# Optimization experiments

Measured on AMD Instinct MI355X. Metric: run time of the kernel, lower is better.

The kernel has to match this reference:

```python
import jax, jax.numpy as jnp
import numpy as np

N_CH = 64          # n_channels
N_HID = 64         # int(ratio * n_inputs), ratio=1, log_diag_cov -> n_inputs = n_channels
N_OUT_CH = 64      # n_out_channels defaults to n_channels
N_MLP_OUT = N_OUT_CH * (N_CH + 1)  # 4160


def setup_inputs() -> dict:
    key = jax.random.key(0)
    k0, k1, k2, k3, k4 = jax.random.split(key, 5)
    x = jax.random.normal(k0, (256, 1, N_CH, 4000), dtype=jnp.float32)
    W1 = jax.random.normal(k1, (N_CH, N_HID), dtype=jnp.float32) * 0.05
    b1 = jax.random.normal(k2, (N_HID,), dtype=jnp.float32) * 0.05
    W2 = jax.random.normal(k3, (N_HID, N_MLP_OUT), dtype=jnp.float32) * 0.05
    b2 = jax.random.normal(k4, (N_MLP_OUT,), dtype=jnp.float32) * 0.05
    return {"x": x, "W1": W1, "b1": b1, "W2": W2, "b2": b2}


def reference(x, W1, b1, W2, b2):
    # x: (B, F, C, T)
    b, f, c, t = x.shape
    # SpatialFeatureExtractor('log_diag_cov'): log of unbiased variance over T
    v = jnp.var(x, axis=3, ddof=1)               # (B, F, C)
    feats = jnp.log(v)
    feats = jnp.where(jnp.isneginf(feats), 0.0, feats)
    # two-layer MLP hypernetwork
    h = jax.nn.relu(feats @ W1 + b1)             # (B, F, H)
    mlp_out = h @ W2 + b2                        # (B, F, n_out_ch*(C+1))
    bias = mlp_out[:, :, :N_OUT_CH].reshape(b, f, N_OUT_CH, 1)
    W = mlp_out[:, :, N_OUT_CH:].reshape(b, f, N_OUT_CH, c)
    # per-sample spatial filter: batched matmul + bias
    out = jnp.einsum('bfoc,bfct->bfot', W, x) + bias  # (B, F, C', T)
    return out.squeeze(1)                        # squeeze_dim1=True, F=1
```

## Files before the change

kernel.cpp:

```cpp
#include <hip/hip_runtime.h>
#include <hip/hip_bf16.h>
#include <cstdint>
#include <math.h>

#define BB 256
#define CC 64
#define TT 4000
#define NHID 64
#define NOUT 64
#define NMLP (NOUT*(CC+1))
#define TCH 128

typedef __attribute__((ext_vector_type(8))) short short8v;
typedef __attribute__((ext_vector_type(4))) float f32x4;

__global__ __launch_bounds__(1024) void k_feat(const float* __restrict__ x,
                                               const float* __restrict__ W1,
                                               const float* __restrict__ b1,
                                               const float* __restrict__ W2,
                                               const float* __restrict__ b2,
                                               __hip_bfloat16* __restrict__ wtg,
                                               float* __restrict__ wsB) {
    int b   = blockIdx.x;
    int tid = threadIdx.x;
    int c   = tid >> 4;
    int sub = tid & 15;

    const float4* row = (const float4*)(x + (size_t)b * (CC * TT) + (size_t)c * TT);
    float s = 0.f, ss = 0.f;
    #pragma unroll 4
    for (int i = sub; i < TT / 4; i += 16) {
        float4 v = row[i];
        s  += v.x + v.y + v.z + v.w;
        ss += v.x * v.x + v.y * v.y + v.z * v.z + v.w * v.w;
    }
    #pragma unroll
    for (int off = 8; off > 0; off >>= 1) {
        s  += __shfl_xor(s, off);
        ss += __shfl_xor(ss, off);
    }

    __shared__ float fs[CC];
    __shared__ float hs[NHID];
    if (sub == 0) {
        float var = (ss - s * s / (float)TT) / (float)(TT - 1);
        float f = logf(var);
        if (isinf(f) && f < 0.f) f = 0.f;
        fs[c] = f;
    }
    __syncthreads();

    if (tid < NHID) {
        float v = b1[tid];
        #pragma unroll 8
        for (int k = 0; k < CC; ++k) v = fmaf(fs[k], W1[k * NHID + tid], v);
        hs[tid] = v > 0.f ? v : 0.f;
    }
    __syncthreads();

    for (int j = tid; j < NMLP; j += 1024) {
        float v = b2[j];
        #pragma unroll 8
        for (int k = 0; k < NHID; ++k) v = fmaf(hs[k], W2[k * NMLP + j], v);
        if (j < NOUT) {
            wsB[b * NOUT + j] = v;
        } else {
            wtg[(size_t)b * 4096 + (j - NOUT)] = __float2bfloat16(v);
        }
    }
}

__global__ __launch_bounds__(256, 4) void k_apply(const float* __restrict__ x,
                                                  const __hip_bfloat16* __restrict__ wtg,
                                                  const float* __restrict__ wsB,
                                                  float* __restrict__ out) {
    int b   = (BB - 1) - blockIdx.y;
    int tb  = blockIdx.x * TCH;
    int tid = threadIdx.x;
    int l   = tid & 63, w = tid >> 6;

    __shared__ unsigned short xt[2][TCH * CC];

    int cslot = tid & 7;
    int f4    = tid >> 3;
    int maxf4 = ((TT - tb) >> 2) - 1;
    int f4c   = f4 <= maxf4 ? f4 : maxf4;
    const float* xb = x + (size_t)b * (CC * TT) + tb + f4c * 4;

    float4 xr[8];
    #pragma unroll
    for (int p = 0; p < 8; ++p)
        xr[p] = *(const float4*)(xb + (size_t)(cslot * 8 + p) * TT);

    #pragma unroll
    for (int j = 0; j < 4; ++j) {
        int t = f4 * 4 + j;
        short8v hv, lv;
        #pragma unroll
        for (int p = 0; p < 8; ++p) {
            float v = (&xr[p].x)[j];
            __hip_bfloat16 h = __float2bfloat16(v);
            unsigned short hu = *(unsigned short*)&h;
            float hf = __uint_as_float((unsigned)hu << 16);
            __hip_bfloat16 lo = __float2bfloat16(v - hf);
            hv[p] = (short)hu;
            lv[p] = (short)*(unsigned short*)&lo;
        }
        int byteoff = t * 128 + ((cslot * 16) ^ ((t & 7) << 4));
        *(short8v*)((char*)&xt[0][0] + byteoff) = hv;
        *(short8v*)((char*)&xt[1][0] + byteoff) = lv;
    }
    __syncthreads();

    const __hip_bfloat16* wb = wtg + (size_t)b * 4096;
    short8v af[4][2];
    #pragma unroll
    for (int mi = 0; mi < 4; ++mi)
        #pragma unroll
        for (int kc = 0; kc < 2; ++kc)
            af[mi][kc] = *(const short8v*)(wb + (mi * 16 + (l & 15)) * 64
                                              + kc * 32 + (l >> 4) * 8);

    f32x4 acc[4][2];
    #pragma unroll
    for (int mi = 0; mi < 4; ++mi) {
        float4 bv = *(const float4*)(wsB + b * 64 + mi * 16 + (l >> 4) * 4);
        #pragma unroll
        for (int ti = 0; ti < 2; ++ti) {
            acc[mi][ti][0] = bv.x; acc[mi][ti][1] = bv.y;
            acc[mi][ti][2] = bv.z; acc[mi][ti][3] = bv.w;
        }
    }

    #pragma unroll
    for (int ti = 0; ti < 2; ++ti) {
        int tl = w * 32 + ti * 16 + (l & 15);
        int rowbase = tl * 128;
        int sw = (tl & 7) << 4;
        short8v bf[2][2];
        #pragma unroll
        for (int kc = 0; kc < 2; ++kc) {
            int boff = rowbase + ((kc * 64 + (l >> 4) * 16) ^ sw);
            bf[kc][0] = *(const short8v*)((const char*)&xt[0][0] + boff);
            bf[kc][1] = *(const short8v*)((const char*)&xt[1][0] + boff);
        }
        #pragma unroll
        for (int mi = 0; mi < 4; ++mi)
            #pragma unroll
            for (int kc = 0; kc < 2; ++kc) {
                acc[mi][ti] = __builtin_amdgcn_mfma_f32_16x16x32_bf16(
                                  af[mi][kc], bf[kc][0], acc[mi][ti], 0, 0, 0);
                acc[mi][ti] = __builtin_amdgcn_mfma_f32_16x16x32_bf16(
                                  af[mi][kc], bf[kc][1], acc[mi][ti], 0, 0, 0);
            }
    }

    __syncthreads();
    float* ot = (float*)&xt[0][0];

    #pragma unroll
    for (int mi = 0; mi < 4; ++mi)
        #pragma unroll
        for (int ti = 0; ti < 2; ++ti) {
            int t = w * 32 + ti * 16 + (l & 15);
            #pragma unroll
            for (int r = 0; r < 4; ++r) {
                int o = mi * 16 + (l >> 4) * 4 + r;
                ot[o * 128 + (t ^ ((o & 7) << 2))] = acc[mi][ti][r];
            }
        }
    __syncthreads();

    int ro = tid >> 3;
    int q0 = tid & 7;
    #pragma unroll
    for (int k2 = 0; k2 < 2; ++k2) {
        int o = ro + k2 * 32;
        int sw = (o & 7) << 2;
        float* op = out + (size_t)b * (NOUT * TT) + (size_t)o * TT + tb;
        #pragma unroll
        for (int kq = 0; kq < 4; ++kq) {
            int t0 = (q0 + kq * 8) * 4;
            if (tb + t0 < TT) {
                f32x4 v = *(const f32x4*)&ot[o * 128 + (t0 ^ sw)];
                __builtin_nontemporal_store(v, (f32x4*)(op + t0));
            }
        }
    }
}

extern "C" void kernel_launch(void* const* d_in, const int* in_sizes, int n_in,
                              void* d_out, int out_size, void* d_ws, size_t ws_size,
                              hipStream_t stream) {
    const float* x  = (const float*)d_in[0];
    const float* W1 = (const float*)d_in[1];
    const float* b1 = (const float*)d_in[2];
    const float* W2 = (const float*)d_in[3];
    const float* b2 = (const float*)d_in[4];
    float* out = (float*)d_out;
    float* ws  = (float*)d_ws;

    float*           wsB = ws;
    __hip_bfloat16*  wtg = (__hip_bfloat16*)(ws + 16384);

    k_feat<<<256, 1024, 0, stream>>>(x, W1, b1, W2, b2, wtg, wsB);
    k_apply<<<dim3(32, 256), 256, 0, stream>>>(x, wtg, wsB, out);
}
```

Measured before the change: 150.3 us.

## Fuse feature MLP and spatial filter apply into one per-batch kernel

Merges the variance/MLP kernel and the MFMA apply kernel into a single 1024-thread block per batch sample. The generated filter weights and bias stay in shared memory instead of going through a global workspace, and four 256-thread sub-groups loop over time chunks, re-reading x that may still be in cache. This removes one launch and the workspace round trip, but it shrinks the grid from 8192 blocks to 256 and uses much more LDS per block, which lowers occupancy and latency hiding.

After: 217.3 us. +44.6%, slower.

```diff
diff --git a/kernel.cpp b/kernel.cpp
--- a/kernel.cpp
+++ b/kernel.cpp
@@ -14,39 +14,43 @@
 typedef __attribute__((ext_vector_type(8))) short short8v;
 typedef __attribute__((ext_vector_type(4))) float f32x4;
 
-__global__ __launch_bounds__(1024) void k_feat(const float* __restrict__ x,
-                                               const float* __restrict__ W1,
-                                               const float* __restrict__ b1,
-                                               const float* __restrict__ W2,
-                                               const float* __restrict__ b2,
-                                               __hip_bfloat16* __restrict__ wtg,
-                                               float* __restrict__ wsB) {
+__global__ __launch_bounds__(1024) void k_fused(const float* __restrict__ x,
+                                                const float* __restrict__ W1,
+                                                const float* __restrict__ b1,
+                                                const float* __restrict__ W2,
+                                                const float* __restrict__ b2,
+                                                float* __restrict__ out) {
     int b   = blockIdx.x;
     int tid = threadIdx.x;
-    int c   = tid >> 4;
-    int sub = tid & 15;
-
-    const float4* row = (const float4*)(x + (size_t)b * (CC * TT) + (size_t)c * TT);
-    float s = 0.f, ss = 0.f;
-    #pragma unroll 4
-    for (int i = sub; i < TT / 4; i += 16) {
-        float4 v = row[i];
-        s  += v.x + v.y + v.z + v.w;
-        ss += v.x * v.x + v.y * v.y + v.z * v.z + v.w * v.w;
-    }
-    #pragma unroll
-    for (int off = 8; off > 0; off >>= 1) {
-        s  += __shfl_xor(s, off);
-        ss += __shfl_xor(ss, off);
-    }
-
+
+    __shared__ unsigned short xt[4][2][TCH * CC];
+    __shared__ unsigned short wl[4096];
+    __shared__ float bl[64];
     __shared__ float fs[CC];
     __shared__ float hs[NHID];
-    if (sub == 0) {
-        float var = (ss - s * s / (float)TT) / (float)(TT - 1);
-        float f = logf(var);
-        if (isinf(f) && f < 0.f) f = 0.f;
-        fs[c] = f;
+
+    {
+        int c   = tid >> 4;
+        int sub = tid & 15;
+        const float4* row = (const float4*)(x + (size_t)b * (CC * TT) + (size_t)c * TT);
+        float s = 0.f, ss = 0.f;
+        #pragma unroll 4
+        for (int i = sub; i < TT / 4; i += 16) {
+            float4 v = row[i];
+            s  += v.x + v.y + v.z + v.w;
+            ss += v.x * v.x + v.y * v.y + v.z * v.z + v.w * v.w;
+        }
+        #pragma unroll
+        for (int off = 8; off > 0; off >>= 1) {
+            s  += __shfl_xor(s, off);
+            ss += __shfl_xor(ss, off);
+        }
+        if (sub == 0) {
+            float var = (ss - s * s / (float)TT) / (float)(TT - 1);
+            float f = logf(var);
+            if (isinf(f) && f < 0.f) f = 0.f;
+            fs[c] = f;
+        }
     }
     __syncthreads();
 
@@ -57,135 +61,140 @@
         hs[tid] = v > 0.f ? v : 0.f;
     }
     __syncthreads();
-
     for (int j = tid; j < NMLP; j += 1024) {
         float v = b2[j];
         #pragma unroll 8
         for (int k = 0; k < NHID; ++k) v = fmaf(hs[k], W2[k * NMLP + j], v);
         if (j < NOUT) {
-            wsB[b * NOUT + j] = v;
+            bl[j] = v;
         } else {
-            wtg[(size_t)b * 4096 + (j - NOUT)] = __float2bfloat16(v);
-        }
-    }
-}
-
-__global__ __launch_bounds__(256, 4) void k_apply(const float* __restrict__ x,
-                                                  const __hip_bfloat16* __restrict__ wtg,
-                                                  const float* __restrict__ wsB,
-                                                  float* __restrict__ out) {
-    int b   = (BB - 1) - blockIdx.y;
-    int tb  = blockIdx.x * TCH;
-    int tid = threadIdx.x;
-    int l   = tid & 63, w = tid >> 6;
-
-    __shared__ unsigned short xt[2][TCH * CC];
-
-    int cslot = tid & 7;
-    int f4    = tid >> 3;
-    int maxf4 = ((TT - tb) >> 2) - 1;
-    int f4c   = f4 <= maxf4 ? f4 : maxf4;
-    const float* xb = x + (size_t)b * (CC * TT) + tb + f4c * 4;
-
-    float4 xr[8];
-    #pragma unroll
-    for (int p = 0; p < 8; ++p)
-        xr[p] = *(const float4*)(xb + (size_t)(cslot * 8 + p) * TT);
-
-    #pragma unroll
-    for (int j = 0; j < 4; ++j) {
-        int t = f4 * 4 + j;
-        short8v hv, lv;
-        #pragma unroll
-        for (int p = 0; p < 8; ++p) {
-            float v = (&xr[p].x)[j];
+            int o = (j - NOUT) >> 6, c = (j - NOUT) & 63;
             __hip_bfloat16 h = __float2bfloat16(v);
-            unsigned short hu = *(unsigned short*)&h;
-            float hf = __uint_as_float((unsigned)hu << 16);
-            __hip_bfloat16 lo = __float2bfloat16(v - hf);
-            hv[p] = (short)hu;
-            lv[p] = (short)*(unsigned short*)&lo;
-        }
-        int byteoff = t * 128 + ((cslot * 16) ^ ((t & 7) << 4));
-        *(short8v*)((char*)&xt[0][0] + byteoff) = hv;
-        *(short8v*)((char*)&xt[1][0] + byteoff) = lv;
+            int byte = o * 128 + ((2 * c) ^ ((o & 7) << 4));
+            *(unsigned short*)((char*)wl + byte) = *(unsigned short*)&h;
+        }
     }
     __syncthreads();
 
-    const __hip_bfloat16* wb = wtg + (size_t)b * 4096;
+    int sb    = tid >> 8;
+    int stid  = tid & 255;
+    int l     = stid & 63;
+    int w     = stid >> 6;
+    int cslot = stid & 7;
+    int f4    = stid >> 3;
+
     short8v af[4][2];
     #pragma unroll
     for (int mi = 0; mi < 4; ++mi)
         #pragma unroll
-        for (int kc = 0; kc < 2; ++kc)
-            af[mi][kc] = *(const short8v*)(wb + (mi * 16 + (l & 15)) * 64
-                                              + kc * 32 + (l >> 4) * 8);
-
-    f32x4 acc[4][2];
-    #pragma unroll
-    for (int mi = 0; mi < 4; ++mi) {
-        float4 bv = *(const float4*)(wsB + b * 64 + mi * 16 + (l >> 4) * 4);
-        #pragma unroll
-        for (int ti = 0; ti < 2; ++ti) {
-            acc[mi][ti][0] = bv.x; acc[mi][ti][1] = bv.y;
-            acc[mi][ti][2] = bv.z; acc[mi][ti][3] = bv.w;
-        }
-    }
-
-    #pragma unroll
-    for (int ti = 0; ti < 2; ++ti) {
-        int tl = w * 32 + ti * 16 + (l & 15);
-        int rowbase = tl * 128;
-        int sw = (tl & 7) << 4;
-        short8v bf[2][2];
-        #pragma unroll
         for (int kc = 0; kc < 2; ++kc) {
-            int boff = rowbase + ((kc * 64 + (l >> 4) * 16) ^ sw);
-            bf[kc][0] = *(const short8v*)((const char*)&xt[0][0] + boff);
-            bf[kc][1] = *(const short8v*)((const char*)&xt[1][0] + boff);
-        }
-        #pragma unroll
-        for (int mi = 0; mi < 4; ++mi)
-            #pragma unroll
-            for (int kc = 0; kc < 2; ++kc) {
-                acc[mi][ti] = __builtin_amdgcn_mfma_f32_16x16x32_bf16(
-                                  af[mi][kc], bf[kc][0], acc[mi][ti], 0, 0, 0);
-                acc[mi][ti] = __builtin_amdgcn_mfma_f32_16x16x32_bf16(
-                                  af[mi][kc], bf[kc][1], acc[mi][ti], 0, 0, 0);
-            }
-    }
-
-    __syncthreads();
-    float* ot = (float*)&xt[0][0];
-
+            int o = mi * 16 + (l & 15);
+            int colbyte = kc * 64 + (l >> 4) * 16;
+            af[mi][kc] = *(const short8v*)((const char*)wl
+                             + o * 128 + (colbyte ^ ((o & 7) << 4)));
+        }
+    float4 bvr[4];
     #pragma unroll
     for (int mi = 0; mi < 4; ++mi)
+        bvr[mi] = *(const float4*)&bl[mi * 16 + (l >> 4) * 4];
+
+    unsigned short* xts = &xt[sb][0][0];
+    unsigned short* xtl = &xt[sb][1][0];
+    float*          ot  = (float*)&xt[sb][0][0];
+
+    #pragma unroll 1
+    for (int it = 0; it < 8; ++it) {
+        int tb = (it * 4 + sb) * TCH;
+
+        int maxf4 = ((TT - tb) >> 2) - 1;
+        int f4c   = f4 <= maxf4 ? f4 : maxf4;
+        const float* xb = x + (size_t)b * (CC * TT) + tb + f4c * 4;
+        float4 xr[8];
+        #pragma unroll
+        for (int p = 0; p < 8; ++p)
+            xr[p] = *(const float4*)(xb + (size_t)(cslot * 8 + p) * TT);
+        #pragma unroll
+        for (int j = 0; j < 4; ++j) {
+            int t = f4 * 4 + j;
+            short8v hv, lv;
+            #pragma unroll
+            for (int p = 0; p < 8; ++p) {
+                float v = (&xr[p].x)[j];
+                __hip_bfloat16 h = __float2bfloat16(v);
+                unsigned short hu = *(unsigned short*)&h;
+                float hf = __uint_as_float((unsigned)hu << 16);
+                __hip_bfloat16 lo2 = __float2bfloat16(v - hf);
+                hv[p] = (short)hu;
+                lv[p] = (short)*(unsigned short*)&lo2;
+            }
+            int byteoff = t * 128 + ((cslot * 16) ^ ((t & 7) << 4));
+            *(short8v*)((char*)xts + byteoff) = hv;
+            *(short8v*)((char*)xtl + byteoff) = lv;
+        }
+        __syncthreads();
+
+        f32x4 acc[4][2];
+        #pragma unroll
+        for (int mi = 0; mi < 4; ++mi)
+            #pragma unroll
+            for (int ti = 0; ti < 2; ++ti) {
+                acc[mi][ti][0] = bvr[mi].x; acc[mi][ti][1] = bvr[mi].y;
+                acc[mi][ti][2] = bvr[mi].z; acc[mi][ti][3] = bvr[mi].w;
+            }
         #pragma unroll
         for (int ti = 0; ti < 2; ++ti) {
-            int t = w * 32 + ti * 16 + (l & 15);
-            #pragma unroll
-            for (int r = 0; r < 4; ++r) {
-                int o = mi * 16 + (l >> 4) * 4 + r;
-                ot[o * 128 + (t ^ ((o & 7) << 2))] = acc[mi][ti][r];
-            }
-        }
-    __syncthreads();
-
-    int ro = tid >> 3;
-    int q0 = tid & 7;
-    #pragma unroll
-    for (int k2 = 0; k2 < 2; ++k2) {
-        int o = ro + k2 * 32;
-        int sw = (o & 7) << 2;
-        float* op = out + (size_t)b * (NOUT * TT) + (size_t)o * TT + tb;
-        #pragma unroll
-        for (int kq = 0; kq < 4; ++kq) {
-            int t0 = (q0 + kq * 8) * 4;
-            if (tb + t0 < TT) {
-                f32x4 v = *(const f32x4*)&ot[o * 128 + (t0 ^ sw)];
-                __builtin_nontemporal_store(v, (f32x4*)(op + t0));
-            }
-        }
+            int tl = w * 32 + ti * 16 + (l & 15);
+            int rowbase = tl * 128;
+            int sw = (tl & 7) << 4;
+            short8v bf[2][2];
+            #pragma unroll
+            for (int kc = 0; kc < 2; ++kc) {
+                int boff = rowbase + ((kc * 64 + (l >> 4) * 16) ^ sw);
+                bf[kc][0] = *(const short8v*)((const char*)xts + boff);
+                bf[kc][1] = *(const short8v*)((const char*)xtl + boff);
+            }
+            #pragma unroll
+            for (int mi = 0; mi < 4; ++mi)
+                #pragma unroll
+                for (int kc = 0; kc < 2; ++kc) {
+                    acc[mi][ti] = __builtin_amdgcn_mfma_f32_16x16x32_bf16(
+                                      af[mi][kc], bf[kc][0], acc[mi][ti], 0, 0, 0);
+                    acc[mi][ti] = __builtin_amdgcn_mfma_f32_16x16x32_bf16(
+                                      af[mi][kc], bf[kc][1], acc[mi][ti], 0, 0, 0);
+                }
+        }
+        __syncthreads();
+
+        #pragma unroll
+        for (int mi = 0; mi < 4; ++mi)
+            #pragma unroll
+            for (int ti = 0; ti < 2; ++ti) {
+                int t = w * 32 + ti * 16 + (l & 15);
+                #pragma unroll
+                for (int r = 0; r < 4; ++r) {
+                    int o = mi * 16 + (l >> 4) * 4 + r;
+                    ot[o * 128 + (t ^ ((o & 7) << 2))] = acc[mi][ti][r];
+                }
+            }
+        __syncthreads();
+
+        int ro = stid >> 3;
+        int q0 = stid & 7;
+        #pragma unroll
+        for (int k2 = 0; k2 < 2; ++k2) {
+            int o = ro + k2 * 32;
+            int sw2 = (o & 7) << 2;
+            float* op = out + (size_t)b * (NOUT * TT) + (size_t)o * TT + tb;
+            #pragma unroll
+            for (int kq = 0; kq < 4; ++kq) {
+                int t0 = (q0 + kq * 8) * 4;
+                if (tb + t0 < TT) {
+                    f32x4 v = *(const f32x4*)&ot[o * 128 + (t0 ^ sw2)];
+                    __builtin_nontemporal_store(v, (f32x4*)(op + t0));
+                }
+            }
+        }
+        __syncthreads();
     }
 }
 
@@ -198,11 +207,6 @@
     const float* W2 = (const float*)d_in[3];
     const float* b2 = (const float*)d_in[4];
     float* out = (float*)d_out;
-    float* ws  = (float*)d_ws;
-
-    float*           wsB = ws;
-    __hip_bfloat16*  wtg = (__hip_bfloat16*)(ws + 16384);
-
-    k_feat<<<256, 1024, 0, stream>>>(x, W1, b1, W2, b2, wtg, wsB);
-    k_apply<<<dim3(32, 256), 256, 0, stream>>>(x, wtg, wsB, out);
+
+    k_fused<<<256, 1024, 0, stream>>>(x, W1, b1, W2, b2, out);
 }
```
